# Optimization experiments

Hardware: AMD Instinct MI355X
Metric: run time of the kernel (lower is better)

Reference implementation:

```python
import jax, jax.numpy as jnp
import numpy as np

N = 50000      # nodes
E = 800000     # edges
D_IN = 128     # embedding_dim
H = 4          # g_num_heads
D = 64         # g_hidden_dim (per head)
SLOPE = 0.2    # g_negative_slope


def setup_inputs() -> dict:
    key = jax.random.key(0)
    ks = jax.random.split(key, 16)
    def lin(k, fin, fout):
        return jax.random.normal(k, (fin, fout), jnp.float32) / np.float32(np.sqrt(fin))
    def att(k, heads):
        return jax.random.normal(k, (heads, D), jnp.float32) * np.float32(0.1)
    return {
        'x':  jax.random.normal(ks[0], (N, D_IN), jnp.float32),
        'src': jax.random.randint(ks[1], (E,), 0, N),
        'dst': jax.random.randint(ks[2], (E,), 0, N),
        'W0': lin(ks[3], D_IN, H * D), 'al0': att(ks[4], H), 'ar0': att(ks[5], H), 'b0': jnp.zeros((H * D,), jnp.float32),
        'W1': lin(ks[6], H * D, H * D), 'al1': att(ks[7], H), 'ar1': att(ks[8], H), 'b1': jnp.zeros((H * D,), jnp.float32),
        'W2': lin(ks[9], H * D, 1 * D), 'al2': att(ks[10], 1), 'ar2': att(ks[11], 1), 'b2': jnp.zeros((D,), jnp.float32),
    }


def gat_layer(x, W, al, ar, b, src, dst, heads, act):
    # x: [N, F_in] -> h: [N, heads, D]
    h = (x @ W).reshape(N, heads, D)
    el = jnp.sum(h * al, axis=-1)                      # [N, heads]
    er = jnp.sum(h * ar, axis=-1)                      # [N, heads]
    e = jax.nn.leaky_relu(el[src] + er[dst], SLOPE)    # [E, heads]
    # edge softmax over incoming edges of each dst node (numerically stable)
    m = jax.ops.segment_max(e, dst, num_segments=N)    # [N, heads]
    ee = jnp.exp(e - m[dst])
    z = jax.ops.segment_sum(ee, dst, num_segments=N)   # [N, heads]
    alpha = ee / z[dst]                                # [E, heads]
    # weighted aggregation of source features
    out = jax.ops.segment_sum(alpha[:, :, None] * h[src], dst, num_segments=N)  # [N, heads, D]
    out = out + b.reshape(1, heads, D)
    return jax.nn.elu(out) if act else out


def reference(x, src, dst, W0, al0, ar0, b0, W1, al1, ar1, b1, W2, al2, ar2, b2):
    f = gat_layer(x, W0, al0, ar0, b0, src, dst, H, True).reshape(N, H * D)
    f = gat_layer(f, W1, al1, ar1, b1, src, dst, H, True).reshape(N, H * D)
    out = gat_layer(f, W2, al2, ar2, b2, src, dst, 1, False).mean(axis=1)  # [N, D]
    return out
```

## Files before the change

kernel.cpp:

```cpp
#include <hip/hip_runtime.h>
#include <math.h>

#define NNODES 50000
#define NEDGES 800000


__global__ void k_zero_int(int* __restrict__ p, int n) {
  int i = blockIdx.x * blockDim.x + threadIdx.x;
  if (i < n) p[i] = 0;
}

__global__ void k_hist(const int* __restrict__ dst, int* __restrict__ deg) {
  int i = blockIdx.x * blockDim.x + threadIdx.x;
  if (i < NEDGES) atomicAdd(&deg[dst[i]], 1);
}

__global__ __launch_bounds__(1024) void k_scan(const int* __restrict__ deg,
                                               int* __restrict__ ptr,
                                               int* __restrict__ cur) {
  __shared__ int s[1024];
  __shared__ int carry;
  const int tid = threadIdx.x;
  if (tid == 0) carry = 0;
  __syncthreads();
  for (int base = 0; base < NNODES; base += 1024) {
    int i = base + tid;
    int v = (i < NNODES) ? deg[i] : 0;
    s[tid] = v;
    __syncthreads();
    for (int off = 1; off < 1024; off <<= 1) {
      int t = (tid >= off) ? s[tid - off] : 0;
      __syncthreads();
      s[tid] += t;
      __syncthreads();
    }
    if (i < NNODES) {
      int e = carry + s[tid] - v;
      ptr[i] = e;
      cur[i] = e;
    }
    __syncthreads();
    if (tid == 0) carry += s[1023];
    __syncthreads();
  }
  if (tid == 0) ptr[NNODES] = carry;
}

__global__ void k_scatter(const int* __restrict__ src, const int* __restrict__ dst,
                          int* __restrict__ cur, int* __restrict__ csr) {
  int i = blockIdx.x * blockDim.x + threadIdx.x;
  if (i < NEDGES) {
    int d = dst[i];
    int p = atomicAdd(&cur[d], 1);
    csr[p] = src[i];
  }
}


template <int K, int NC>
__global__ __launch_bounds__(256) void k_gemm(const float* __restrict__ A,
                                              const float* __restrict__ B,
                                              float* __restrict__ C) {
  __shared__ float As[64][17];
  __shared__ float Bs[16][64];
  const int tid = threadIdx.x;
  const int tx = tid & 15;
  const int ty = tid >> 4;
  const int rowBase = blockIdx.x * 64;
  const int colBase = blockIdx.y * 64;
  const int arow = tid >> 2;
  const int acol = (tid & 3) << 2;
  const int brow = tid >> 4;
  const int bcol = (tid & 15) << 2;

  float acc[4][4] = {};
  for (int k0 = 0; k0 < K; k0 += 16) {
    float4 av = make_float4(0.f, 0.f, 0.f, 0.f);
    int gr = rowBase + arow;
    if (gr < NNODES) av = *(const float4*)&A[(size_t)gr * K + k0 + acol];
    As[arow][acol + 0] = av.x;
    As[arow][acol + 1] = av.y;
    As[arow][acol + 2] = av.z;
    As[arow][acol + 3] = av.w;
    float4 bv = *(const float4*)&B[(size_t)(k0 + brow) * NC + colBase + bcol];
    *(float4*)&Bs[brow][bcol] = bv;
    __syncthreads();
#pragma unroll
    for (int k = 0; k < 16; ++k) {
      float4 b4 = *(const float4*)&Bs[k][tx << 2];
#pragma unroll
      for (int i = 0; i < 4; ++i) {
        float a = As[(ty << 2) + i][k];
        acc[i][0] = fmaf(a, b4.x, acc[i][0]);
        acc[i][1] = fmaf(a, b4.y, acc[i][1]);
        acc[i][2] = fmaf(a, b4.z, acc[i][2]);
        acc[i][3] = fmaf(a, b4.w, acc[i][3]);
      }
    }
    __syncthreads();
  }
#pragma unroll
  for (int i = 0; i < 4; ++i) {
    int r = rowBase + (ty << 2) + i;
    if (r < NNODES) {
      float4 o = make_float4(acc[i][0], acc[i][1], acc[i][2], acc[i][3]);
      *(float4*)&C[(size_t)r * NC + colBase + (tx << 2)] = o;
    }
  }
}


template <int HEADS>
__global__ __launch_bounds__(HEADS * 64) void k_elr(const float* __restrict__ h,
                                                    const float* __restrict__ al,
                                                    const float* __restrict__ ar,
                                                    float* __restrict__ el,
                                                    float* __restrict__ er) {
  const int n = blockIdx.x;
  const int tid = threadIdx.x;
  float hv = h[(size_t)n * HEADS * 64 + tid];
  float pl = hv * al[tid];
  float pr = hv * ar[tid];
#pragma unroll
  for (int m = 1; m < 64; m <<= 1) {
    pl += __shfl_xor(pl, m);
    pr += __shfl_xor(pr, m);
  }
  if ((tid & 63) == 0) {
    el[n * HEADS + (tid >> 6)] = pl;
    er[n * HEADS + (tid >> 6)] = pr;
  }
}


template <int HEADS, bool ACT>
__global__ __launch_bounds__(64) void k_aggregate(const float* __restrict__ h,
                                                  const float* __restrict__ el,
                                                  const float* __restrict__ er,
                                                  const int* __restrict__ ptr,
                                                  const int* __restrict__ csr,
                                                  const float* __restrict__ bias,
                                                  float* __restrict__ out) {
  constexpr int HD = HEADS * 64;
  constexpr int VEC = HEADS;
  constexpr int CH = 64 / HEADS;
  const int n = blockIdx.x;
  const int tid = threadIdx.x;
  const int head = tid / (64 / HEADS);
  const int beg = ptr[n];
  const int deg = ptr[n + 1] - beg;

  __shared__ float s_m[HEADS];
  __shared__ float s_z[HEADS];
  __shared__ int s_src[CH];
  __shared__ float s_w[64];

  {
    const int hh = tid & (HEADS - 1);
    const float ern = er[n * HEADS + hh];
    float mloc = -INFINITY;
    for (int i = tid / HEADS; i < deg; i += 64 / HEADS) {
      int s = csr[beg + i];
      float e = el[s * HEADS + hh] + ern;
      e = e > 0.f ? e : 0.2f * e;
      mloc = fmaxf(mloc, e);
    }
#pragma unroll
    for (int m = HEADS; m < 64; m <<= 1) mloc = fmaxf(mloc, __shfl_xor(mloc, m));
    float zloc = 0.f;
    for (int i = tid / HEADS; i < deg; i += 64 / HEADS) {
      int s = csr[beg + i];
      float e = el[s * HEADS + hh] + ern;
      e = e > 0.f ? e : 0.2f * e;
      zloc += expf(e - mloc);
    }
#pragma unroll
    for (int m = HEADS; m < 64; m <<= 1) zloc += __shfl_xor(zloc, m);
    if (tid < HEADS) { s_m[tid] = mloc; s_z[tid] = zloc; }
  }
  __syncthreads();
  const float invz = (deg > 0) ? 1.0f / s_z[head] : 0.f;

  float acc[VEC];
#pragma unroll
  for (int v = 0; v < VEC; ++v) acc[v] = 0.f;

  for (int c0 = 0; c0 < deg; c0 += CH) {
    const int cnt = min(CH, deg - c0);
    __syncthreads();
    {
      const int c = tid / HEADS;
      const int hh = tid & (HEADS - 1);
      if (c < cnt) {
        int s = csr[beg + c0 + c];
        if (hh == 0) s_src[c] = s;
        float e = el[s * HEADS + hh] + er[n * HEADS + hh];
        e = e > 0.f ? e : 0.2f * e;
        s_w[tid] = expf(e - s_m[hh]);
      }
    }
    __syncthreads();
    for (int c = 0; c < cnt; ++c) {
      const float w = s_w[c * HEADS + head];
      const float* hp = &h[(size_t)s_src[c] * HD + tid * VEC];
      if constexpr (VEC == 4) {
        float4 hv = *(const float4*)hp;
        acc[0] = fmaf(w, hv.x, acc[0]);
        acc[1] = fmaf(w, hv.y, acc[1]);
        acc[2] = fmaf(w, hv.z, acc[2]);
        acc[3] = fmaf(w, hv.w, acc[3]);
      } else {
        acc[0] = fmaf(w, hp[0], acc[0]);
      }
    }
  }

#pragma unroll
  for (int v = 0; v < VEC; ++v) {
    float r = acc[v] * invz + bias[tid * VEC + v];
    if (ACT) r = r > 0.f ? r : expm1f(r);
    acc[v] = r;
  }
  if constexpr (VEC == 4) {
    float4 o = make_float4(acc[0], acc[1], acc[2], acc[3]);
    *(float4*)&out[(size_t)n * HD + (tid << 2)] = o;
  } else {
    out[(size_t)n * HD + tid] = acc[0];
  }
}


extern "C" void kernel_launch(void* const* d_in, const int* in_sizes, int n_in,
                              void* d_out, int out_size, void* d_ws, size_t ws_size,
                              hipStream_t stream) {
  const float* x   = (const float*)d_in[0];
  const int*   src = (const int*)d_in[1];
  const int*   dst = (const int*)d_in[2];
  const float* W0  = (const float*)d_in[3];
  const float* al0 = (const float*)d_in[4];
  const float* ar0 = (const float*)d_in[5];
  const float* b0  = (const float*)d_in[6];
  const float* W1  = (const float*)d_in[7];
  const float* al1 = (const float*)d_in[8];
  const float* ar1 = (const float*)d_in[9];
  const float* b1  = (const float*)d_in[10];
  const float* W2  = (const float*)d_in[11];
  const float* al2 = (const float*)d_in[12];
  const float* ar2 = (const float*)d_in[13];
  const float* b2  = (const float*)d_in[14];
  float* out = (float*)d_out;

  float* hA = (float*)d_ws;
  float* fB = hA + (size_t)NNODES * 256;
  float* el = fB + (size_t)NNODES * 256;
  float* er = el + (size_t)NNODES * 4;
  int* deg  = (int*)(er + (size_t)NNODES * 4);
  int* ptr  = deg + NNODES;
  int* cur  = ptr + NNODES + 1;
  int* csr  = cur + NNODES;

  k_zero_int<<<(NNODES + 255) / 256, 256, 0, stream>>>(deg, NNODES);
  k_hist<<<(NEDGES + 255) / 256, 256, 0, stream>>>(dst, deg);
  k_scan<<<1, 1024, 0, stream>>>(deg, ptr, cur);
  k_scatter<<<(NEDGES + 255) / 256, 256, 0, stream>>>(src, dst, cur, csr);

  dim3 g0((NNODES + 63) / 64, 256 / 64);
  k_gemm<128, 256><<<g0, 256, 0, stream>>>(x, W0, hA);
  k_elr<4><<<NNODES, 256, 0, stream>>>(hA, al0, ar0, el, er);
  k_aggregate<4, true><<<NNODES, 64, 0, stream>>>(hA, el, er, ptr, csr, b0, fB);
  k_gemm<256, 256><<<g0, 256, 0, stream>>>(fB, W1, hA);
  k_elr<4><<<NNODES, 256, 0, stream>>>(hA, al1, ar1, el, er);
  k_aggregate<4, true><<<NNODES, 64, 0, stream>>>(hA, el, er, ptr, csr, b1, fB);
  dim3 g2((NNODES + 63) / 64, 1);
  k_gemm<256, 64><<<g2, 256, 0, stream>>>(fB, W2, hA);
  k_elr<1><<<NNODES, 64, 0, stream>>>(hA, al2, ar2, el, er);
  k_aggregate<1, false><<<NNODES, 64, 0, stream>>>(hA, el, er, ptr, csr, b2, out);
}
```

Measured before the change: 799.4 us.

## Enlarge GEMM register tiles and use wavefront-shuffle scan for CSR offsets

The GEMM moves from 64x64 tiles with a 4x4 per-thread micro-tile to 128x128 (or 128x64) tiles with an 8x8 (or 8x4) micro-tile. A is stored transposed in shared memory so it can be read with float4 loads. This raises arithmetic intensity per shared-memory load and cuts global reloads of B, at the cost of more registers and fewer blocks. Separately, the single-block degree scan replaces the shared-memory Hillis-Steele loop, with its many barriers, by wavefront shuffle scans plus a small per-wave prefix.

Result: faster. 753.2 us (-5.8%).

```diff
diff --git a/kernel.cpp b/kernel.cpp
--- a/kernel.cpp
+++ b/kernel.cpp
@@ -18,32 +18,46 @@
 __global__ __launch_bounds__(1024) void k_scan(const int* __restrict__ deg,
                                                int* __restrict__ ptr,
                                                int* __restrict__ cur) {
-  __shared__ int s[1024];
-  __shared__ int carry;
+  __shared__ int s_w[16];
+  __shared__ int s_carry;
   const int tid = threadIdx.x;
-  if (tid == 0) carry = 0;
+  const int lane = tid & 63;
+  const int wid = tid >> 6;
+  if (tid == 0) s_carry = 0;
   __syncthreads();
   for (int base = 0; base < NNODES; base += 1024) {
-    int i = base + tid;
-    int v = (i < NNODES) ? deg[i] : 0;
-    s[tid] = v;
-    __syncthreads();
-    for (int off = 1; off < 1024; off <<= 1) {
-      int t = (tid >= off) ? s[tid - off] : 0;
-      __syncthreads();
-      s[tid] += t;
-      __syncthreads();
-    }
+    const int i = base + tid;
+    const int v = (i < NNODES) ? deg[i] : 0;
+    int x = v;
+#pragma unroll
+    for (int off = 1; off < 64; off <<= 1) {
+      int t = __shfl_up(x, off);
+      if (lane >= off) x += t;
+    }
+    if (lane == 63) s_w[wid] = x;
+    __syncthreads();
+    const int carry = s_carry;
+    if (wid == 0) {
+      int ws = (lane < 16) ? s_w[lane] : 0;
+#pragma unroll
+      for (int off = 1; off < 16; off <<= 1) {
+        int t = __shfl_up(ws, off);
+        if (lane >= off) ws += t;
+      }
+      if (lane < 16) s_w[lane] = ws;
+    }
+    __syncthreads();
+    const int woff = (wid > 0) ? s_w[wid - 1] : 0;
+    const int excl = carry + woff + (x - v);
     if (i < NNODES) {
-      int e = carry + s[tid] - v;
-      ptr[i] = e;
-      cur[i] = e;
-    }
-    __syncthreads();
-    if (tid == 0) carry += s[1023];
-    __syncthreads();
-  }
-  if (tid == 0) ptr[NNODES] = carry;
+      ptr[i] = excl;
+      cur[i] = excl;
+    }
+    __syncthreads();
+    if (tid == 0) s_carry = carry + s_w[15];
+  }
+  __syncthreads();
+  if (tid == 0) ptr[NNODES] = s_carry;
 }
 
 __global__ void k_scatter(const int* __restrict__ src, const int* __restrict__ dst,
@@ -57,54 +71,82 @@
 }
 
 
-template <int K, int NC>
+template <int K, int NC, int BN>
 __global__ __launch_bounds__(256) void k_gemm(const float* __restrict__ A,
                                               const float* __restrict__ B,
                                               float* __restrict__ C) {
-  __shared__ float As[64][17];
-  __shared__ float Bs[16][64];
+  constexpr int BM = 128;
+  constexpr int BK = 16;
+  constexpr int TN = BN / 16;
+  __shared__ float Ast[BK][BM + 4];
+  __shared__ float Bs[BK][BN];
   const int tid = threadIdx.x;
   const int tx = tid & 15;
   const int ty = tid >> 4;
-  const int rowBase = blockIdx.x * 64;
-  const int colBase = blockIdx.y * 64;
+  const int rowBase = blockIdx.x * BM;
+  const int colBase = blockIdx.y * BN;
   const int arow = tid >> 2;
-  const int acol = (tid & 3) << 2;
-  const int brow = tid >> 4;
-  const int bcol = (tid & 15) << 2;
-
-  float acc[4][4] = {};
-  for (int k0 = 0; k0 < K; k0 += 16) {
-    float4 av = make_float4(0.f, 0.f, 0.f, 0.f);
-    int gr = rowBase + arow;
-    if (gr < NNODES) av = *(const float4*)&A[(size_t)gr * K + k0 + acol];
-    As[arow][acol + 0] = av.x;
-    As[arow][acol + 1] = av.y;
-    As[arow][acol + 2] = av.z;
-    As[arow][acol + 3] = av.w;
-    float4 bv = *(const float4*)&B[(size_t)(k0 + brow) * NC + colBase + bcol];
-    *(float4*)&Bs[brow][bcol] = bv;
-    __syncthreads();
-#pragma unroll
-    for (int k = 0; k < 16; ++k) {
-      float4 b4 = *(const float4*)&Bs[k][tx << 2];
-#pragma unroll
-      for (int i = 0; i < 4; ++i) {
-        float a = As[(ty << 2) + i][k];
-        acc[i][0] = fmaf(a, b4.x, acc[i][0]);
-        acc[i][1] = fmaf(a, b4.y, acc[i][1]);
-        acc[i][2] = fmaf(a, b4.z, acc[i][2]);
-        acc[i][3] = fmaf(a, b4.w, acc[i][3]);
-      }
-    }
-    __syncthreads();
-  }
-#pragma unroll
-  for (int i = 0; i < 4; ++i) {
-    int r = rowBase + (ty << 2) + i;
+  const int ak = (tid & 3) << 2;
+
+  float acc[8][TN] = {};
+
+  for (int k0 = 0; k0 < K; k0 += BK) {
+#pragma unroll
+    for (int rr = 0; rr < 2; ++rr) {
+      const int r = arow + rr * 64;
+      const int gr = rowBase + r;
+      float4 av = make_float4(0.f, 0.f, 0.f, 0.f);
+      if (gr < NNODES) av = *(const float4*)&A[(size_t)gr * K + k0 + ak];
+      Ast[ak + 0][r] = av.x;
+      Ast[ak + 1][r] = av.y;
+      Ast[ak + 2][r] = av.z;
+      Ast[ak + 3][r] = av.w;
+    }
+    if constexpr (BN == 128) {
+      const int brow = tid >> 5;
+      const int bcol = (tid & 31) << 2;
+#pragma unroll
+      for (int rr = 0; rr < 2; ++rr)
+        *(float4*)&Bs[brow + rr * 8][bcol] =
+            *(const float4*)&B[(size_t)(k0 + brow + rr * 8) * NC + colBase + bcol];
+    } else {
+      const int brow = tid >> 4;
+      const int bcol = (tid & 15) << 2;
+      *(float4*)&Bs[brow][bcol] =
+          *(const float4*)&B[(size_t)(k0 + brow) * NC + colBase + bcol];
+    }
+    __syncthreads();
+#pragma unroll
+    for (int k = 0; k < BK; ++k) {
+      float4 a0 = *(const float4*)&Ast[k][ty * 8];
+      float4 a1 = *(const float4*)&Ast[k][ty * 8 + 4];
+      float a[8] = {a0.x, a0.y, a0.z, a0.w, a1.x, a1.y, a1.z, a1.w};
+      float b[TN];
+      float4 b0 = *(const float4*)&Bs[k][tx * 4];
+      b[0] = b0.x; b[1] = b0.y; b[2] = b0.z; b[3] = b0.w;
+      if constexpr (TN == 8) {
+        float4 b1 = *(const float4*)&Bs[k][64 + tx * 4];
+        b[4] = b1.x; b[5] = b1.y; b[6] = b1.z; b[7] = b1.w;
+      }
+#pragma unroll
+      for (int i = 0; i < 8; ++i)
+#pragma unroll
+        for (int j = 0; j < TN; ++j) acc[i][j] = fmaf(a[i], b[j], acc[i][j]);
+    }
+    __syncthreads();
+  }
+#pragma unroll
+  for (int i = 0; i < 8; ++i) {
+    const int r = rowBase + ty * 8 + i;
     if (r < NNODES) {
-      float4 o = make_float4(acc[i][0], acc[i][1], acc[i][2], acc[i][3]);
-      *(float4*)&C[(size_t)r * NC + colBase + (tx << 2)] = o;
+      {
+        float4 o = make_float4(acc[i][0], acc[i][1], acc[i][2], acc[i][3]);
+        *(float4*)&C[(size_t)r * NC + colBase + tx * 4] = o;
+      }
+      if constexpr (TN == 8) {
+        float4 o = make_float4(acc[i][4], acc[i][5], acc[i][6], acc[i][7]);
+        *(float4*)&C[(size_t)r * NC + colBase + 64 + tx * 4] = o;
+      }
     }
   }
 }
@@ -264,15 +306,15 @@
   k_scan<<<1, 1024, 0, stream>>>(deg, ptr, cur);
   k_scatter<<<(NEDGES + 255) / 256, 256, 0, stream>>>(src, dst, cur, csr);
 
-  dim3 g0((NNODES + 63) / 64, 256 / 64);
-  k_gemm<128, 256><<<g0, 256, 0, stream>>>(x, W0, hA);
+  dim3 g128((NNODES + 127) / 128, 256 / 128);
+  k_gemm<128, 256, 128><<<g128, 256, 0, stream>>>(x, W0, hA);
   k_elr<4><<<NNODES, 256, 0, stream>>>(hA, al0, ar0, el, er);
   k_aggregate<4, true><<<NNODES, 64, 0, stream>>>(hA, el, er, ptr, csr, b0, fB);
-  k_gemm<256, 256><<<g0, 256, 0, stream>>>(fB, W1, hA);
+  k_gemm<256, 256, 128><<<g128, 256, 0, stream>>>(fB, W1, hA);
   k_elr<4><<<NNODES, 256, 0, stream>>>(hA, al1, ar1, el, er);
   k_aggregate<4, true><<<NNODES, 64, 0, stream>>>(hA, el, er, ptr, csr, b1, fB);
-  dim3 g2((NNODES + 63) / 64, 1);
-  k_gemm<256, 64><<<g2, 256, 0, stream>>>(fB, W2, hA);
+  dim3 g2((NNODES + 127) / 128, 1);
+  k_gemm<256, 64, 64><<<g2, 256, 0, stream>>>(fB, W2, hA);
   k_elr<1><<<NNODES, 64, 0, stream>>>(hA, al2, ar2, el, er);
   k_aggregate<1, false><<<NNODES, 64, 0, stream>>>(hA, el, er, ptr, csr, b2, out);
 }
```
